# Performance work log

Measured on AMD Instinct MI355X. Metric: run time of the kernel, lower is better.

Reference implementation:

```python
import jax, jax.numpy as jnp
import numpy as np

# Production GravNet config: 8 events x 4096 hits, K=40 neighbours, 4 spatial dims
B, V, K, S, P, F_IN, F_OUT = 8, 4096, 40, 4, 64, 64, 128
N = B * V
MAX_RADIUS_SQ = 1.0  # SelectKnn(max_radius=1.0)


def setup_inputs() -> dict:
    key = jax.random.key(0)
    ks = jax.random.split(key, 7)
    x = jax.random.normal(ks[0], (N, F_IN), jnp.float32)
    # Dense layer params (glorot-ish scaling)
    W_prop = jax.random.normal(ks[1], (F_IN, P), jnp.float32) / np.sqrt(F_IN)
    b_prop = jnp.zeros((P,), jnp.float32)
    W_sp = jax.random.normal(ks[2], (F_IN, S), jnp.float32) / np.sqrt(F_IN)
    b_sp = jnp.zeros((S,), jnp.float32)
    # output transform input dim = n_prop_total (2*P) + F_IN
    W_out = jax.random.normal(ks[3], (2 * P + F_IN, F_OUT), jnp.float32) / np.sqrt(2 * P + F_IN)
    b_out = jnp.zeros((F_OUT,), jnp.float32)
    row_splits = jnp.arange(B + 1, dtype=jnp.int32) * V  # equal-size ragged segments
    return dict(x=x, W_prop=W_prop, b_prop=b_prop, W_sp=W_sp, b_sp=b_sp,
                W_out=W_out, b_out=b_out, row_splits=row_splits)


def _knn_indices(coords):
    """Per-event brute-force KNN. coords: [N,S] -> global neighbour idx [N,K]."""
    c = coords.reshape(B, V, S)
    # pairwise squared distances within each event: [B,V,V]
    d = jnp.sum((c[:, :, None, :] - c[:, None, :, :]) ** 2, axis=-1)
    neg_d, idx = jax.lax.top_k(-d, K + 1)  # nearest first; col 0 is self (d=0)
    idx, dsq = idx[:, :, 1:], -neg_d[:, :, 1:]
    # tf_compatible max_radius: out-of-radius neighbours -> self index
    self_idx = jnp.arange(V, dtype=idx.dtype)[None, :, None]
    idx = jnp.where(dsq > MAX_RADIUS_SQ, self_idx, idx)
    gidx = idx + (jnp.arange(B, dtype=idx.dtype) * V)[:, None, None]
    return gidx.reshape(N, K)


def reference(x, W_prop, b_prop, W_sp, b_sp, W_out, b_out, row_splits):
    coords = x @ W_sp + b_sp                      # [N,S] learned coordinates
    nidx = _knn_indices(coords)                   # [N,K] (int, non-diff)
    nb_coords = coords[nidx]                      # [N,K,S] gather
    dsq = jnp.sum((coords[:, None, :] - nb_coords) ** 2, axis=-1)  # [N,K]
    feat = x @ W_prop + b_prop                    # [N,P]
    w = jnp.exp(-10.0 * dsq)[:, :, None]          # gauss_of_lin(10*d^2)
    nf = feat[nidx] * w                           # [N,K,P]
    agg = jnp.concatenate([nf.max(axis=1), nf.mean(axis=1)], axis=-1)  # [N,2P]
    out = jnp.tanh(jnp.concatenate([agg, x], axis=-1) @ W_out + b_out)  # [N,F_OUT]
    return out
```

## Files before the change

### kernel.cpp

```cpp
#include <hip/hip_runtime.h>
#include <cstdint>
#include <cstddef>

#define NB   8
#define VV   4096
#define KNN  40
#define NTOT 32768
#define CAP  224
#define INFB 0x7F800000u
#define ONEB 0x3F800000u

__device__ __forceinline__ int slabf(float x) {
  int b = (int)floorf((x + 4.f) * 2.f);
  return b < 0 ? 0 : (b > 15 ? 15 : b);
}
__device__ __forceinline__ int ybf(float y) {
  int b = (int)floorf((y + 4.f) * 4.f);
  return b < 0 ? 0 : (b > 31 ? 31 : b);
}

__global__ __launch_bounds__(256) void k_prep(
    const float* __restrict__ x, const float* __restrict__ W_prop,
    const float* __restrict__ b_prop, const float* __restrict__ W_sp,
    const float* __restrict__ b_sp, const float* __restrict__ W_out,
    float* __restrict__ coords, float* __restrict__ feat,
    float* __restrict__ xW, int* __restrict__ hist)
{
  __shared__ float xt[64][64];
  const int t = threadIdx.x;
  const int row0 = blockIdx.x * 64;

  #pragma unroll
  for (int i = 0; i < 16; ++i) {
    int idx = t + i * 256;
    xt[idx >> 6][idx & 63] = x[(size_t)row0 * 64 + idx];
  }
  __syncthreads();

  {
    const int col = t & 63, rb = (t >> 6) * 16;
    float acc[16];
    #pragma unroll
    for (int i = 0; i < 16; ++i) acc[i] = b_prop[col];
    for (int k = 0; k < 64; k += 4) {
      const float w0 = W_prop[(k + 0) * 64 + col];
      const float w1 = W_prop[(k + 1) * 64 + col];
      const float w2 = W_prop[(k + 2) * 64 + col];
      const float w3 = W_prop[(k + 3) * 64 + col];
      #pragma unroll
      for (int i = 0; i < 16; ++i) {
        const float4 a4 = *(const float4*)&xt[rb + i][k];
        acc[i] += a4.x * w0 + a4.y * w1 + a4.z * w2 + a4.w * w3;
      }
    }
    #pragma unroll
    for (int i = 0; i < 16; ++i)
      feat[(size_t)(row0 + rb + i) * 64 + col] = acc[i];
  }

  {
    const int col = t & 127, who = t >> 7;
    #pragma unroll
    for (int p = 0; p < 2; ++p) {
      const int rb = who * 16 + p * 32;
      float acc[16];
      #pragma unroll
      for (int i = 0; i < 16; ++i) acc[i] = 0.f;
      for (int k = 0; k < 64; k += 4) {
        const float w0 = W_out[(size_t)(128 + k + 0) * 128 + col];
        const float w1 = W_out[(size_t)(128 + k + 1) * 128 + col];
        const float w2 = W_out[(size_t)(128 + k + 2) * 128 + col];
        const float w3 = W_out[(size_t)(128 + k + 3) * 128 + col];
        #pragma unroll
        for (int i = 0; i < 16; ++i) {
          const float4 a4 = *(const float4*)&xt[rb + i][k];
          acc[i] += a4.x * w0 + a4.y * w1 + a4.z * w2 + a4.w * w3;
        }
      }
      #pragma unroll
      for (int i = 0; i < 16; ++i)
        xW[(size_t)(row0 + rb + i) * 128 + col] = acc[i];
    }
  }

  if (t < 64) {
    float a0 = b_sp[0], a1 = b_sp[1], a2 = b_sp[2], a3 = b_sp[3];
    for (int k = 0; k < 64; ++k) {
      const float xv = xt[t][k];
      a0 += xv * W_sp[k * 4 + 0];
      a1 += xv * W_sp[k * 4 + 1];
      a2 += xv * W_sp[k * 4 + 2];
      a3 += xv * W_sp[k * 4 + 3];
    }
    ((float4*)coords)[row0 + t] = make_float4(a0, a1, a2, a3);
    const int ev = (row0 + t) >> 12;
    atomicAdd(&hist[ev * 512 + slabf(a0) * 32 + ybf(a1)], 1);
  }
}

__global__ __launch_bounds__(512) void k_scatter(
    const float* __restrict__ coords, float* __restrict__ csort,
    unsigned short* __restrict__ perm, const int* __restrict__ hist,
    int* __restrict__ cursorDelta, unsigned short* __restrict__ prefg)
{
  __shared__ int pref[513];
  const int t = threadIdx.x;
  const int ev = blockIdx.x >> 3;
  const int i = ((blockIdx.x & 7) << 9) + t;
  const int evbase = ev * VV;

  if (t < 64) {
    const int l = t;
    const int* h = hist + ev * 512 + 8 * l;
    int hv[8], s = 0;
    #pragma unroll
    for (int j = 0; j < 8; ++j) { hv[j] = h[j]; s += hv[j]; }
    int incl = s;
    #pragma unroll
    for (int off = 1; off < 64; off <<= 1) {
      const int v = __shfl_up(incl, off);
      if (l >= off) incl += v;
    }
    int run = incl - s;
    #pragma unroll
    for (int j = 0; j < 8; ++j) { pref[8 * l + j] = run; run += hv[j]; }
    if (l == 63) pref[512] = run;
  }
  __syncthreads();

  const float4 c = ((const float4*)coords)[evbase + i];
  const int key = slabf(c.x) * 32 + ybf(c.y);
  const int pos = pref[key] + atomicAdd(&cursorDelta[ev * 512 + key], 1);
  ((float4*)csort)[evbase + pos] = c;
  perm[evbase + pos] = (unsigned short)i;

  if ((blockIdx.x & 7) == 0) {
    prefg[ev * 513 + t] = (unsigned short)pref[t];
    if (t == 0) prefg[ev * 513 + 512] = (unsigned short)pref[512];
  }
}

template <int NC>
__device__ __forceinline__ unsigned bs40(const uint2* __restrict__ list,
                                         int M, int lane) {
  unsigned dv[NC];
  #pragma unroll
  for (int j = 0; j < NC; ++j) {
    const int e = lane + j * 64;
    dv[j] = (e < M) ? list[e].x : INFB;
  }
  unsigned lo = 0, hi = ONEB;
  while (lo < hi) {
    const unsigned mid = (lo + hi) >> 1;
    int cnt = 0;
    #pragma unroll
    for (int j = 0; j < NC; ++j)
      cnt += (int)__popcll(__ballot(dv[j] <= mid));
    if (cnt >= KNN) hi = mid; else lo = mid + 1;
  }
  return hi;
}

#define AGG_CHUNK(J0, N)                                                     \
  {                                                                          \
    float fv[N], wgt[N];                                                     \
    _Pragma("unroll")                                                        \
    for (int j = 0; j < N; ++j) {                                            \
      const uint2 en = list[(J0) + j];                                       \
      wgt[j] = __expf(-10.f * __uint_as_float(en.x));                        \
      const int ei = __builtin_amdgcn_readfirstlane((int)en.y);              \
      fv[j] = fe[(size_t)ei * 64 + lane];                                    \
    }                                                                        \
    _Pragma("unroll")                                                        \
    for (int j = 0; j < N; ++j) {                                            \
      const float v = fv[j] * wgt[j];                                        \
      vmax = fmaxf(vmax, v);                                                 \
      vsum += v;                                                             \
    }                                                                        \
  }

__global__ __launch_bounds__(512, 4) void k_knn(
    const float* __restrict__ coords,
    const unsigned short* __restrict__ perm,
    const unsigned short* __restrict__ prefg,
    const float* __restrict__ feat, float* __restrict__ agg)
{
  __shared__ float4 cs[VV];
  __shared__ uint2 lists[8][CAP];
  __shared__ unsigned short pr[513];

  const int t = threadIdx.x, lane = t & 63;
  const int wvid = __builtin_amdgcn_readfirstlane(t) >> 6;
  const int bid0 = blockIdx.x;
  const int bid = (bid0 & 7) * 64 + (bid0 >> 3);
  const int ev = bid >> 6;
  const int slot = bid & 63;
  const int evbase = ev * VV;

  {
    const float4* cg = (const float4*)coords + evbase;
    for (int i = t; i < VV; i += 512) cs[i] = cg[i];
    for (int i = t; i < 513; i += 512) pr[i] = prefg[ev * 513 + i];
  }
  __syncthreads();

  uint2* list = lists[wvid];
  const float* fe = feat + (size_t)evbase * 64;
  const unsigned long long lmask = (1ull << lane) - 1ull;

  auto scanAll = [&](unsigned rbits, int q, float4 qc,
                     int slo, int shi, int yblo, int ybhi) -> int {
    int M = 0, pend = 0;
    for (int s = slo; s <= shi; ++s) {
      int alo = ((int)pr[(s << 5) + yblo]) & ~63;
      int ahi = (((int)pr[(s << 5) + ybhi + 1]) + 63) & ~63;
      alo = alo < pend ? pend : alo;
      if (ahi < alo) ahi = alo;
      pend = ahi;
      #pragma unroll 4
      for (int base = alo; base < ahi; base += 64) {
        const int c = base + lane;
        const float4 cc = cs[c];
        const float dx = qc.x - cc.x, dy = qc.y - cc.y;
        const float dz = qc.z - cc.z, dw = qc.w - cc.w;
        const float dsq = dx * dx + dy * dy + dz * dz + dw * dw;
        const bool pred = (__float_as_uint(dsq) <= rbits) && (c != q);
        const unsigned long long bm = __ballot(pred);
        if (pred) {
          const int pos = M + (int)__popcll(bm & lmask);
          if (pos < CAP)
            list[pos] = make_uint2(__float_as_uint(dsq), (unsigned)c);
        }
        M += (int)__popcll(bm);
      }
    }
    return M;
  };

  for (int qi = 0; qi < 8; ++qi) {
    const int q = slot + (qi * 8 + wvid) * 64;
    const float4 qc = cs[q];
    const int origq = (int)perm[evbase + q];
    const int slo = slabf(qc.x - 1.f), shi = slabf(qc.x + 1.f);
    const int yblo = ybf(qc.y - 1.f),  ybhi = ybf(qc.y + 1.f);

    int M = scanAll(ONEB, q, qc, slo, shi, yblo, ybhi);
    bool ok = true;

    if (M > CAP) {
      const unsigned t0 = bs40<4>(list, CAP, lane);
      M = scanAll(t0, q, qc, slo, shi, yblo, ybhi);
      ok = (M <= CAP);
    }

    float vmax = -__builtin_inff(), vsum = 0.f;

    if (ok) {
      for (int be = 0; be < M; be += 64) {
        const int e = be + lane;
        if (e < M) {
          uint2 en = list[e];
          en.y = (unsigned)perm[evbase + (int)en.y];
          list[e] = en;
        }
      }

      int Msel;
      if (M > KNN) {
        unsigned taub;
        if      (M <=  64) taub = bs40<1>(list, M, lane);
        else if (M <= 128) taub = bs40<2>(list, M, lane);
        else               taub = bs40<4>(list, M, lane);
        int S = 0;
        for (int be = 0; be < M; be += 64) {
          const int e = be + lane;
          uint2 en = make_uint2(0u, 0u);
          bool p = false;
          if (e < M) { en = list[e]; p = (en.x <= taub); }
          const unsigned long long bm = __ballot(p);
          if (p) list[S + (int)__popcll(bm & lmask)] = en;
          S += (int)__popcll(bm);
        }
        Msel = S;
      } else {
        if (lane >= M && lane < KNN)
          list[lane] = make_uint2(0u, (unsigned)origq);
        Msel = KNN;
      }

      if (Msel == KNN) {
        AGG_CHUNK(0, 16)
        AGG_CHUNK(16, 16)
        AGG_CHUNK(32, 8)
      } else {
        #pragma unroll 4
        for (int e = 0; e < Msel; ++e) {
          const uint2 en = list[e];
          const int ei = __builtin_amdgcn_readfirstlane((int)en.y);
          const float w = __expf(-10.f * __uint_as_float(en.x));
          const float v = fe[(size_t)ei * 64 + lane] * w;
          vmax = fmaxf(vmax, v);
          vsum += v;
        }
      }
    } else {
      unsigned lo = 0, hi = ONEB;
      while (lo < hi) {
        const unsigned mid = (lo + hi) >> 1;
        const float fm = __uint_as_float(mid);
        int cnt = 0, pend = 0;
        for (int s = slo; s <= shi; ++s) {
          int alo = ((int)pr[(s << 5) + yblo]) & ~63;
          int ahi = (((int)pr[(s << 5) + ybhi + 1]) + 63) & ~63;
          alo = alo < pend ? pend : alo;
          if (ahi < alo) ahi = alo;
          pend = ahi;
          for (int base = alo; base < ahi; base += 64) {
            const int c = base + lane;
            const float4 cc = cs[c];
            const float dx = qc.x - cc.x, dy = qc.y - cc.y;
            const float dz = qc.z - cc.z, dw = qc.w - cc.w;
            const float dsq = dx * dx + dy * dy + dz * dz + dw * dw;
            cnt += (int)__popcll(__ballot(dsq <= fm && c != q));
          }
        }
        if (cnt >= KNN) hi = mid; else lo = mid + 1;
      }
      const float tau = __uint_as_float(hi);
      int pend = 0;
      for (int s = slo; s <= shi; ++s) {
        int alo = ((int)pr[(s << 5) + yblo]) & ~63;
        int ahi = (((int)pr[(s << 5) + ybhi + 1]) + 63) & ~63;
        alo = alo < pend ? pend : alo;
        if (ahi < alo) ahi = alo;
        pend = ahi;
        for (int c = alo; c < ahi; ++c) {
          if (c == q) continue;
          const float4 cc = cs[c];
          const float dx = qc.x - cc.x, dy = qc.y - cc.y;
          const float dz = qc.z - cc.z, dw = qc.w - cc.w;
          const float dsq = dx * dx + dy * dy + dz * dz + dw * dw;
          if (dsq <= tau) {
            const int ei = (int)perm[evbase + c];
            const float w = __expf(-10.f * dsq);
            const float v = fe[(size_t)ei * 64 + lane] * w;
            vmax = fmaxf(vmax, v);
            vsum += v;
          }
        }
      }
    }

    const int g = evbase + origq;
    agg[(size_t)g * 128 + lane]      = vmax;
    agg[(size_t)g * 128 + 64 + lane] = vsum * (1.f / 40.f);
  }
}

__global__ __launch_bounds__(256) void k_out(
    const float* __restrict__ agg, const float* __restrict__ W_out,
    const float* __restrict__ b_out, float* __restrict__ out)
{
  __shared__ float at[64][128];
  const int t = threadIdx.x;
  const int row0 = blockIdx.x * 64;

  #pragma unroll
  for (int i = 0; i < 32; ++i) {
    int idx = t + i * 256;
    at[idx >> 7][idx & 127] = agg[(size_t)row0 * 128 + idx];
  }
  __syncthreads();

  const int col = t & 127, who = t >> 7;
  #pragma unroll
  for (int p = 0; p < 2; ++p) {
    const int rb = who * 16 + p * 32;
    float acc[16];
    #pragma unroll
    for (int i = 0; i < 16; ++i) acc[i] = 0.f;
    for (int k = 0; k < 128; k += 4) {
      const float w0 = W_out[(size_t)(k + 0) * 128 + col];
      const float w1 = W_out[(size_t)(k + 1) * 128 + col];
      const float w2 = W_out[(size_t)(k + 2) * 128 + col];
      const float w3 = W_out[(size_t)(k + 3) * 128 + col];
      #pragma unroll
      for (int i = 0; i < 16; ++i) {
        const float4 a4 = *(const float4*)&at[rb + i][k];
        acc[i] += a4.x * w0 + a4.y * w1 + a4.z * w2 + a4.w * w3;
      }
    }
    const float bb = b_out[col];
    #pragma unroll
    for (int i = 0; i < 16; ++i) {
      const size_t o = (size_t)(row0 + rb + i) * 128 + col;
      float v = acc[i] + bb + out[o];
      v = fminf(15.f, fmaxf(-15.f, v));
      const float e = __expf(2.f * v);
      out[o] = (e - 1.f) / (e + 1.f);
    }
  }
}

extern "C" void kernel_launch(void* const* d_in, const int* in_sizes, int n_in,
                              void* d_out, int out_size, void* d_ws, size_t ws_size,
                              hipStream_t stream) {
  const float* x      = (const float*)d_in[0];
  const float* W_prop = (const float*)d_in[1];
  const float* b_prop = (const float*)d_in[2];
  const float* W_sp   = (const float*)d_in[3];
  const float* b_sp   = (const float*)d_in[4];
  const float* W_out  = (const float*)d_in[5];
  const float* b_out  = (const float*)d_in[6];

  float* out = (float*)d_out;
  char* ws = (char*)d_ws;
  float* coords          = (float*)(ws);
  float* csort           = (float*)(ws + (512 << 10));
  float* feat            = (float*)(ws + (1 << 20));
  float* agg             = (float*)(ws + (9 << 20));
  unsigned short* perm   = (unsigned short*)(ws + (25 << 20));
  unsigned short* prefg  = (unsigned short*)(ws + (25 << 20) + 65536);
  int* hist              = (int*)(ws + (25 << 20) + 65536 + 8704);
  int* cursorDelta       = (int*)(ws + (25 << 20) + 65536 + 8704 + 16384);

  hipMemsetAsync(hist, 0, 32768, stream);
  k_prep<<<NTOT / 64, 256, 0, stream>>>(x, W_prop, b_prop, W_sp, b_sp, W_out,
                                        coords, feat, out ,
                                        hist);
  k_scatter<<<NB * 8, 512, 0, stream>>>(coords, csort, perm, hist,
                                        cursorDelta, prefg);
  k_knn<<<NB * (VV / 64), 512, 0, stream>>>(csort, perm, prefg, feat, agg);
  k_out<<<NTOT / 64, 256, 0, stream>>>(agg, W_out, b_out, out);
}
```

Before: 184.2 us.

## Fuse output projection and tanh into the KNN aggregation kernel

Removes the separate k_out launch and runs the 128x128 output projection, bias, residual add and tanh at the end of k_knn. Each block records the original indices of its 64 queries, rereads their agg rows from global memory into the now-free coordinate shared buffer, and does the matmul there. This saves one kernel launch and lets the agg reads likely hit in cache. In exchange, k_knn gains register pressure and an extra tail phase with only 512 blocks, and output rows are written scattered by original index.

After: 180.0 us. -2.3%, faster.

```diff
diff --git a/kernel.cpp b/kernel.cpp
--- a/kernel.cpp
+++ b/kernel.cpp
@@ -166,10 +166,10 @@
     float fv[N], wgt[N];                                                     \
     _Pragma("unroll")                                                        \
     for (int j = 0; j < N; ++j) {                                            \
-      const uint2 en = list[(J0) + j];                                       \
+      const uint2 en = list[(J0) + j];              \
       wgt[j] = __expf(-10.f * __uint_as_float(en.x));                        \
       const int ei = __builtin_amdgcn_readfirstlane((int)en.y);              \
-      fv[j] = fe[(size_t)ei * 64 + lane];                                    \
+      fv[j] = fe[(size_t)ei * 64 + lane];        \
     }                                                                        \
     _Pragma("unroll")                                                        \
     for (int j = 0; j < N; ++j) {                                            \
@@ -183,11 +183,14 @@
     const float* __restrict__ coords,
     const unsigned short* __restrict__ perm,
     const unsigned short* __restrict__ prefg,
-    const float* __restrict__ feat, float* __restrict__ agg)
+    const float* __restrict__ feat, float* __restrict__ agg,
+    const float* __restrict__ W_out, const float* __restrict__ b_out,
+    float* __restrict__ out)
 {
   __shared__ float4 cs[VV];
   __shared__ uint2 lists[8][CAP];
   __shared__ unsigned short pr[513];
+  __shared__ unsigned short origq_s[64];
 
   const int t = threadIdx.x, lane = t & 63;
   const int wvid = __builtin_amdgcn_readfirstlane(t) >> 6;
@@ -241,6 +244,7 @@
     const int q = slot + (qi * 8 + wvid) * 64;
     const float4 qc = cs[q];
     const int origq = (int)perm[evbase + q];
+    if (lane == 0) origq_s[qi * 8 + wvid] = (unsigned short)origq;
     const int slo = slabf(qc.x - 1.f), shi = slabf(qc.x + 1.f);
     const int yblo = ybf(qc.y - 1.f),  ybhi = ybf(qc.y + 1.f);
 
@@ -355,27 +359,20 @@
     agg[(size_t)g * 128 + lane]      = vmax;
     agg[(size_t)g * 128 + 64 + lane] = vsum * (1.f / 40.f);
   }
-}
-
-__global__ __launch_bounds__(256) void k_out(
-    const float* __restrict__ agg, const float* __restrict__ W_out,
-    const float* __restrict__ b_out, float* __restrict__ out)
-{
-  __shared__ float at[64][128];
-  const int t = threadIdx.x;
-  const int row0 = blockIdx.x * 64;
-
+
+  __syncthreads();
+  float* aggS = (float*)cs;
   #pragma unroll
-  for (int i = 0; i < 32; ++i) {
-    int idx = t + i * 256;
-    at[idx >> 7][idx & 127] = agg[(size_t)row0 * 128 + idx];
+  for (int p = 0; p < 4; ++p) {
+    const int idx = t + p * 512;
+    const int row = idx >> 5, seg = idx & 31;
+    const int g = evbase + (int)origq_s[row];
+    ((float4*)aggS)[idx] = *(const float4*)&agg[(size_t)g * 128 + seg * 4];
   }
   __syncthreads();
 
-  const int col = t & 127, who = t >> 7;
-  #pragma unroll
-  for (int p = 0; p < 2; ++p) {
-    const int rb = who * 16 + p * 32;
+  {
+    const int col = t & 127, who = t >> 7;
     float acc[16];
     #pragma unroll
     for (int i = 0; i < 16; ++i) acc[i] = 0.f;
@@ -386,14 +383,15 @@
       const float w3 = W_out[(size_t)(k + 3) * 128 + col];
       #pragma unroll
       for (int i = 0; i < 16; ++i) {
-        const float4 a4 = *(const float4*)&at[rb + i][k];
+        const float4 a4 = *(const float4*)&aggS[(who * 16 + i) * 128 + k];
         acc[i] += a4.x * w0 + a4.y * w1 + a4.z * w2 + a4.w * w3;
       }
     }
     const float bb = b_out[col];
     #pragma unroll
     for (int i = 0; i < 16; ++i) {
-      const size_t o = (size_t)(row0 + rb + i) * 128 + col;
+      const int row = who * 16 + i;
+      const size_t o = ((size_t)evbase + origq_s[row]) * 128 + col;
       float v = acc[i] + bb + out[o];
       v = fminf(15.f, fmaxf(-15.f, v));
       const float e = __expf(2.f * v);
@@ -430,6 +428,6 @@
                                         hist);
   k_scatter<<<NB * 8, 512, 0, stream>>>(coords, csort, perm, hist,
                                         cursorDelta, prefg);
-  k_knn<<<NB * (VV / 64), 512, 0, stream>>>(csort, perm, prefg, feat, agg);
-  k_out<<<NTOT / 64, 256, 0, stream>>>(agg, W_out, b_out, out);
-}
+  k_knn<<<NB * (VV / 64), 512, 0, stream>>>(csort, perm, prefg, feat, agg,
+                                            W_out, b_out, out);
+}
```
